# Kernel optimization log

Measured on AMD Instinct MI355X. Metric: run time of the kernel, lower is better.

## Reference

```python
import jax, jax.numpy as jnp
import numpy as np


def setup_inputs() -> dict:
    key = jax.random.key(0)
    k1, k2, k3, k4 = jax.random.split(key, 4)
    B, N, D, P = 1, 8192, 128, 2  # batch must be 1 (see .view(B,N,N) in source)
    x = jax.random.normal(k1, (B, N, D), dtype=jnp.float32)
    points = jax.random.normal(k2, (B, N, P), dtype=jnp.float32)
    # nn.Linear params, stored as (in, out) so y = x @ W + b
    W1 = jax.random.normal(k3, (2 * D, 2 * D), dtype=jnp.float32) * 0.04
    b1 = jnp.zeros((2 * D,), dtype=jnp.float32)
    W2 = jax.random.normal(k4, (2 * D, D), dtype=jnp.float32) * 0.04
    b2 = jnp.zeros((D,), dtype=jnp.float32)
    return {"x": x, "points": points, "W1": W1, "b1": b1, "W2": W2, "b2": b2, "K": 16}


def reference(x, points, W1, b1, W2, b2, K):
    B, N, _ = points.shape
    D = x.shape[-1]
    # torch.cdist on flattened (B*N, P) points, reshaped to (B, N, N)
    # (valid only for B == 1, matching the original module). Squared distance
    # is monotone in Euclidean distance, so top-k indices are identical.
    pf = points.reshape(B * N, -1)
    sq = jnp.sum(pf * pf, axis=-1)
    d2 = sq[:, None] + sq[None, :] - 2.0 * (pf @ pf.T)  # (BN, BN)
    d2 = d2.reshape(B, N, N)
    # topk(-dist, K+1) -> nearest K+1 (self first), drop self
    _, idx = jax.lax.top_k(-d2, K + 1)  # (B, N, K+1)
    idx = idx[:, :, 1:]  # (B, N, K)
    # gather neighbor features: knn_fts[b, n, k] = x[b, idx[b, n, k]]
    knn = x[jnp.arange(B)[:, None, None], idx]  # (B, N, K, D)
    center = jnp.broadcast_to(x[:, :, None, :], (B, N, K, D))
    local = jnp.concatenate([knn - center, center], axis=-1)  # (B, N, K, 2D)
    h = jax.nn.gelu(local @ W1 + b1, approximate=False)
    h = jax.nn.gelu(h @ W2 + b2, approximate=False)
    return jnp.mean(h, axis=2)  # (B, N, D)
```

## Files before the change

### kernel.cpp

```cpp
#include <hip/hip_runtime.h>

typedef __attribute__((ext_vector_type(8))) short short8;
typedef __attribute__((ext_vector_type(4))) float f32x4;

__device__ __forceinline__ unsigned short f2bf(float f) {
    unsigned int u = __float_as_uint(f);
    unsigned int r = u + 0x7fffu + ((u >> 16) & 1u);
    return (unsigned short)(r >> 16);
}

__device__ __forceinline__ float bf2f(short s) {
    return __uint_as_float(((unsigned int)(unsigned short)s) << 16);
}

__device__ __forceinline__ float gelu_fast(float v) {
    float x2 = v * v;
    float s  = v * fmaf(-0.102943195f, x2, -2.3022077f);
    float e  = __builtin_amdgcn_exp2f(s);
    return v * __builtin_amdgcn_rcpf(1.0f + e);
}

__device__ __forceinline__ unsigned int d2key(float d2) {
    unsigned int u = __float_as_uint(d2);
    return u ^ (((unsigned int)(((int)u) >> 31)) | 0x80000000u);
}

#define U64MAX 0xFFFFFFFFFFFFFFFFull

#define D2_FROM_Q(px, py, XI, YI, SQI)                                           \
    ({ const float sqj_ = __fadd_rn(__fmul_rn((px), (px)), __fmul_rn((py), (py))); \
       const float t_   = fmaf((YI), (py), __fmul_rn((XI), (px)));                 \
       const float s_   = __fadd_rn((SQI), sqj_);                                  \
       fmaf(-2.0f, t_, s_); })

__device__ __forceinline__ float bitonic64f(float v, int lane) {
#pragma unroll
    for (int k = 2; k <= 64; k <<= 1) {
#pragma unroll
        for (int j = k >> 1; j > 0; j >>= 1) {
            float pv = __shfl_xor(v, j, 64);
            const bool up  = ((lane & k) == 0);
            const bool low = ((lane & j) == 0);
            const float mn = fminf(v, pv);
            const float mx = fmaxf(v, pv);
            v = (up == low) ? mn : mx;
        }
    }
    return v;
}

__device__ __forceinline__ void insert_cand(
        unsigned long long* crow, int* cnt,
        float px, float py, float XI, float YI, float SQI, int i) {
    const float d2 = D2_FROM_Q(px, py, XI, YI, SQI);
    const unsigned int key = d2key(d2);
    int pos = atomicAdd(cnt, 1);
    if (pos < 128)
        crow[pos] = ((unsigned long long)key << 32) | (unsigned int)i;
}

#define KNN_SLACK 2.0e-3f

__global__ __launch_bounds__(256) void knn_kernel(
        const float* __restrict__ points,
        const float* __restrict__ W1, const float* __restrict__ W2,
        unsigned short* __restrict__ W1t, unsigned short* __restrict__ W2t,
        int* __restrict__ idx_out) {
    __shared__ float pmin[4][4][64];
    __shared__ float tshr[4];
    __shared__ unsigned long long cand[4][128];
    __shared__ int ccnt[4];

    const int bid = blockIdx.x;
    const int tid = threadIdx.x;

    if (bid < 384) {
        int g = bid * 256 + tid;
        if (g < 65536) {
            int d = g >> 8, c = g & 255;
            W1t[c * 256 + d] = f2bf(W1[g]);
        } else if (g < 98304) {
            int g2 = g - 65536;
            int d = g2 >> 7, c = g2 & 127;
            W2t[c * 256 + d] = f2bf(W2[g2]);
        }
        return;
    }

    const int wv    = tid >> 6;
    const int lane  = tid & 63;
    const int qbase = (bid - 384) << 2;

    float xi[4], yi[4], sqi_[4], n2x[4], n2y[4];
#pragma unroll
    for (int t = 0; t < 4; ++t) {
        xi[t] = points[(qbase + t) * 2 + 0];
        yi[t] = points[(qbase + t) * 2 + 1];
        sqi_[t] = __fadd_rn(__fmul_rn(xi[t], xi[t]), __fmul_rn(yi[t], yi[t]));
        n2x[t] = -2.0f * xi[t];
        n2y[t] = -2.0f * yi[t];
    }

    const float4* p4 = (const float4*)points;
    const float4* pw = p4 + wv * 1024 + lane;

    if (tid < 4) ccnt[tid] = 0;

    float vmn[4] = {1e30f, 1e30f, 1e30f, 1e30f};
#pragma unroll 4
    for (int j = 0; j < 16; ++j) {
        const float4 pp = pw[j * 64];
        const float sqa = fmaf(pp.x, pp.x, pp.y * pp.y);
        const float sqb = fmaf(pp.z, pp.z, pp.w * pp.w);
#pragma unroll
        for (int t = 0; t < 4; ++t) {
            const float da = fmaf(n2x[t], pp.x, fmaf(n2y[t], pp.y, sqa));
            const float db = fmaf(n2x[t], pp.z, fmaf(n2y[t], pp.w, sqb));
            vmn[t] = fminf(fminf(da, db), vmn[t]);
        }
    }
#pragma unroll
    for (int t = 0; t < 4; ++t) pmin[t][wv][lane] = vmn[t];
    __syncthreads();

    {
        const int q = wv;
        const float m = fminf(fminf(pmin[q][0][lane], pmin[q][1][lane]),
                              fminf(pmin[q][2][lane], pmin[q][3][lane]));
        const float s = bitonic64f(m, lane);
        if (lane == 16) tshr[q] = s + KNN_SLACK;
    }
    __syncthreads();
    float Ta[4];
#pragma unroll
    for (int t = 0; t < 4; ++t) Ta[t] = tshr[t];

#pragma unroll 4
    for (int j = 0; j < 16; ++j) {
        const float4 pp = pw[j * 64];
        const int i0 = (wv * 1024 + j * 64 + lane) * 2;
        const float sqa = fmaf(pp.x, pp.x, pp.y * pp.y);
        const float sqb = fmaf(pp.z, pp.z, pp.w * pp.w);
#pragma unroll
        for (int t = 0; t < 4; ++t) {
            const float da = fmaf(n2x[t], pp.x, fmaf(n2y[t], pp.y, sqa));
            const float db = fmaf(n2x[t], pp.z, fmaf(n2y[t], pp.w, sqb));
            if (fminf(da, db) <= Ta[t]) {
                if (da <= Ta[t])
                    insert_cand(cand[t], &ccnt[t],
                                pp.x, pp.y, xi[t], yi[t], sqi_[t], i0);
                if (db <= Ta[t])
                    insert_cand(cand[t], &ccnt[t],
                                pp.z, pp.w, xi[t], yi[t], sqi_[t], i0 + 1);
            }
        }
    }
    __syncthreads();

    {
        const int q = qbase + wv;
        const unsigned long long* candw = cand[wv];
        const int cc = ccnt[wv];
        const int n = cc < 128 ? cc : 128;
        const unsigned long long c0 = (lane < n)      ? candw[lane]      : U64MAX;
        const unsigned long long c1 = (lane + 64 < n) ? candw[lane + 64] : U64MAX;
        int r0 = 0, r1 = 0;
        for (int mI = 0; mI < n; ++mI) {
            const unsigned long long cm = candw[mI];
            r0 += (cm < c0) ? 1 : 0;
            r1 += (cm < c1) ? 1 : 0;
        }
        if (lane < n && r0 >= 1 && r0 <= 16)
            idx_out[q * 16 + r0 - 1] = (int)(unsigned int)(c0 & 0xFFFFFFFFull);
        if (lane + 64 < n && r1 >= 1 && r1 <= 16)
            idx_out[q * 16 + r1 - 1] = (int)(unsigned int)(c1 & 0xFFFFFFFFull);
    }
}

__global__ __launch_bounds__(256) void gemmAD_kernel(
        const float* __restrict__ x, const unsigned short* __restrict__ W1t,
        const float* __restrict__ b1,
        unsigned short* __restrict__ Abf, unsigned short* __restrict__ Dbf) {
    __shared__ unsigned short sx[64 * 136];
    __shared__ unsigned short tA[64 * 68];
    __shared__ unsigned short tD[64 * 68];
    const int tid = threadIdx.x;
    const int rb  = (blockIdx.x >> 2) * 64;
    const int cb  = (blockIdx.x & 3) * 64;

    {
        const int r   = ((tid >> 6) << 4) | (tid & 15);
        const int seg = (tid >> 4) & 3;
        const float* xr = x + (rb + r) * 128 + seg * 32;
        unsigned short* dst = sx + r * 136 + seg * 32;
#pragma unroll
        for (int u = 0; u < 8; ++u) {
            float4 a = ((const float4*)xr)[u];
            uint2 w;
            w.x = (unsigned)f2bf(a.x) | ((unsigned)f2bf(a.y) << 16);
            w.y = (unsigned)f2bf(a.z) | ((unsigned)f2bf(a.w) << 16);
            *(uint2*)(dst + u * 4) = w;
        }
    }
    __syncthreads();

    const int lane = tid & 63, wv = tid >> 6;
    const int m = lane & 15, quad = lane >> 4;
    const int ko0 = quad * 8;

    f32x4 accA[4], accC[4];
#pragma unroll
    for (int i = 0; i < 4; ++i) { accA[i] = (f32x4){0,0,0,0}; accC[i] = (f32x4){0,0,0,0}; }

    const int colL = wv * 16 + m;

#pragma unroll
    for (int ks = 0; ks < 4; ++ks) {
        const int ko = ks * 32 + ko0;
        short8 af[4];
#pragma unroll
        for (int rt = 0; rt < 4; ++rt)
            af[rt] = *(const short8*)(sx + (rt * 16 + m) * 136 + ko);
        const unsigned short* wp = W1t + (cb + colL) * 256 + ko;
        const short8 bA = *(const short8*)(wp);
        const short8 bC = *(const short8*)(wp + 128);
#pragma unroll
        for (int rt = 0; rt < 4; ++rt) {
            accA[rt] = __builtin_amdgcn_mfma_f32_16x16x32_bf16(af[rt], bA, accA[rt], 0, 0, 0);
            accC[rt] = __builtin_amdgcn_mfma_f32_16x16x32_bf16(af[rt], bC, accC[rt], 0, 0, 0);
        }
    }

    {
        const float bias = b1[cb + colL];
#pragma unroll
        for (int rt = 0; rt < 4; ++rt)
#pragma unroll
            for (int j = 0; j < 4; ++j) {
                const int rowL = rt * 16 + quad * 4 + j;
                float a = accA[rt][j];
                float d = accC[rt][j] - a + bias;
                tA[rowL * 68 + colL] = f2bf(a);
                tD[rowL * 68 + colL] = f2bf(d);
            }
    }
    __syncthreads();

    {
        const int r  = tid >> 2;
        const int sg = tid & 3;
        const unsigned short* sa = tA + r * 68 + sg * 16;
        const unsigned short* sd = tD + r * 68 + sg * 16;
        unsigned short* da = Abf + (rb + r) * 256 + cb + sg * 16;
        unsigned short* dd = Dbf + (rb + r) * 256 + cb + sg * 16;
        *(short8*)(da)     = *(const short8*)(sa);
        *(short8*)(da + 8) = *(const short8*)(sa + 8);
        *(short8*)(dd)     = *(const short8*)(sd);
        *(short8*)(dd + 8) = *(const short8*)(sd + 8);
    }
}

__global__ __launch_bounds__(256) void mlp_kernel(
        const unsigned short* __restrict__ Abf, const unsigned short* __restrict__ Dbf,
        const unsigned short* __restrict__ W2t, const float* __restrict__ b2,
        const int* __restrict__ idx, float* __restrict__ out) {
    __shared__ unsigned short sh[64 * 264];
    const int tid = threadIdx.x;
    const int qb  = blockIdx.x << 2;

    {
        const int r   = ((tid >> 6) << 4) | (tid & 15);
        const int seg = (tid >> 4) & 3;
        const int gq  = qb + (r >> 4);
        const int nb  = idx[(gq << 4) + (r & 15)];
        const unsigned short* arow = Abf + nb * 256 + seg * 64;
        const unsigned short* drow = Dbf + gq * 256 + seg * 64;
        unsigned short* dst = sh + r * 264 + seg * 64;
#pragma unroll
        for (int u = 0; u < 8; ++u) {
            short8 av = *(const short8*)(arow + u * 8);
            short8 dv = *(const short8*)(drow + u * 8);
            short8 hv;
#pragma unroll
            for (int e = 0; e < 8; ++e) {
                float h = bf2f(av[e]) + bf2f(dv[e]);
                hv[e] = (short)f2bf(gelu_fast(h));
            }
            *(short8*)(dst + u * 8) = hv;
        }
    }
    __syncthreads();

    const int lane = tid & 63, wv = tid >> 6;
    const int m = lane & 15, quad = lane >> 4;
    const int ko0 = quad * 8;

    f32x4 acc2[8];
#pragma unroll
    for (int i = 0; i < 8; ++i) acc2[i] = (f32x4){0.f, 0.f, 0.f, 0.f};
#pragma unroll
    for (int ks = 0; ks < 8; ++ks) {
        const int ko = ks * 32 + ko0;
        short8 af[4], bfr[2];
#pragma unroll
        for (int rt = 0; rt < 4; ++rt)
            af[rt] = *(const short8*)(sh + (rt * 16 + m) * 264 + ko);
#pragma unroll
        for (int ct = 0; ct < 2; ++ct)
            bfr[ct] = *(const short8*)(W2t + (wv * 32 + ct * 16 + m) * 256 + ko);
#pragma unroll
        for (int rt = 0; rt < 4; ++rt)
#pragma unroll
            for (int ct = 0; ct < 2; ++ct)
                acc2[rt * 2 + ct] = __builtin_amdgcn_mfma_f32_16x16x32_bf16(
                    af[rt], bfr[ct], acc2[rt * 2 + ct], 0, 0, 0);
    }

#pragma unroll
    for (int ct = 0; ct < 2; ++ct) {
        const int col = wv * 32 + ct * 16 + m;
        const float bias = b2[col];
#pragma unroll
        for (int rt = 0; rt < 4; ++rt) {
            float s = 0.f;
#pragma unroll
            for (int j = 0; j < 4; ++j)
                s += gelu_fast(acc2[rt * 2 + ct][j] + bias);
            s += __shfl_xor(s, 16, 64);
            s += __shfl_xor(s, 32, 64);
            if (quad == 0) out[(qb + rt) * 128 + col] = s * 0.0625f;
        }
    }
}

extern "C" void kernel_launch(void* const* d_in, const int* in_sizes, int n_in,
                              void* d_out, int out_size, void* d_ws, size_t ws_size,
                              hipStream_t stream) {
    const float* x      = (const float*)d_in[0];
    const float* points = (const float*)d_in[1];
    const float* W1     = (const float*)d_in[2];
    const float* b1     = (const float*)d_in[3];
    const float* W2     = (const float*)d_in[4];
    const float* b2     = (const float*)d_in[5];
    float* out = (float*)d_out;

    char* ws = (char*)d_ws;
    unsigned short* W1t = (unsigned short*)ws;
    unsigned short* W2t = (unsigned short*)(ws + 131072);
    int*            idx = (int*)(ws + 196608);
    unsigned short* Abf = (unsigned short*)(ws + 720896);
    unsigned short* Dbf = (unsigned short*)(ws + 4915200);

    knn_kernel<<<2432, 256, 0, stream>>>(points, W1, W2, W1t, W2t, idx);
    gemmAD_kernel<<<512, 256, 0, stream>>>(x, W1t, b1, Abf, Dbf);
    mlp_kernel<<<2048, 256, 0, stream>>>(Abf, Dbf, W2t, b2, idx, out);
}
```

Measured before the change: 131.5 us.

## Fuse first-layer GEMM into KNN kernel launch, reading W1 directly in fp32

Merges the x@W1 GEMM blocks into the KNN kernel as extra block ranges, removing one kernel launch and letting the GEMM run concurrently with the neighbor search. The W1 transpose-to-bf16 staging is dropped: each lane now gathers fp32 W1 elements with strided loads and converts them inline. Outputs are written straight to global memory without the shared-memory transpose, so stores are uncoalesced. The shared memory is reused across the block roles through a single union buffer.

```diff
diff --git a/kernel.cpp b/kernel.cpp
--- a/kernel.cpp
+++ b/kernel.cpp
@@ -61,35 +61,100 @@
 
 #define KNN_SLACK 2.0e-3f
 
-__global__ __launch_bounds__(256) void knn_kernel(
-        const float* __restrict__ points,
+__global__ __launch_bounds__(256) void fused_kernel(
+        const float* __restrict__ points, const float* __restrict__ x,
         const float* __restrict__ W1, const float* __restrict__ W2,
-        unsigned short* __restrict__ W1t, unsigned short* __restrict__ W2t,
+        const float* __restrict__ b1,
+        unsigned short* __restrict__ W2t,
+        unsigned short* __restrict__ Abf, unsigned short* __restrict__ Dbf,
         int* __restrict__ idx_out) {
-    __shared__ float pmin[4][4][64];
-    __shared__ float tshr[4];
-    __shared__ unsigned long long cand[4][128];
-    __shared__ int ccnt[4];
+    __shared__ unsigned long long smem8[2192];
 
     const int bid = blockIdx.x;
     const int tid = threadIdx.x;
 
-    if (bid < 384) {
-        int g = bid * 256 + tid;
-        if (g < 65536) {
-            int d = g >> 8, c = g & 255;
-            W1t[c * 256 + d] = f2bf(W1[g]);
-        } else if (g < 98304) {
-            int g2 = g - 65536;
-            int d = g2 >> 7, c = g2 & 127;
-            W2t[c * 256 + d] = f2bf(W2[g2]);
+    if (bid < 512) {
+        unsigned short* sx = (unsigned short*)smem8;
+        const int rb = (bid >> 2) * 64;
+        const int cb = (bid & 3) * 64;
+
+        {
+            const int r   = ((tid >> 6) << 4) | (tid & 15);
+            const int seg = (tid >> 4) & 3;
+            const float* xr = x + (rb + r) * 128 + seg * 32;
+            unsigned short* dst = sx + r * 136 + seg * 32;
+#pragma unroll
+            for (int u = 0; u < 8; ++u) {
+                float4 a = ((const float4*)xr)[u];
+                uint2 w;
+                w.x = (unsigned)f2bf(a.x) | ((unsigned)f2bf(a.y) << 16);
+                w.y = (unsigned)f2bf(a.z) | ((unsigned)f2bf(a.w) << 16);
+                *(uint2*)(dst + u * 4) = w;
+            }
+        }
+        __syncthreads();
+
+        const int lane = tid & 63, wv = tid >> 6;
+        const int m = lane & 15, quad = lane >> 4;
+        const int ko0 = quad * 8;
+
+        f32x4 accA[4], accC[4];
+#pragma unroll
+        for (int i = 0; i < 4; ++i) { accA[i] = (f32x4){0,0,0,0}; accC[i] = (f32x4){0,0,0,0}; }
+
+        const int gc = cb + wv * 16 + m;
+
+#pragma unroll
+        for (int ks = 0; ks < 4; ++ks) {
+            const int ko = ks * 32 + ko0;
+            short8 af[4];
+#pragma unroll
+            for (int rt = 0; rt < 4; ++rt)
+                af[rt] = *(const short8*)(sx + (rt * 16 + m) * 136 + ko);
+            short8 bA, bC;
+#pragma unroll
+            for (int e = 0; e < 8; ++e) {
+                bA[e] = (short)f2bf(W1[(ko + e) * 256 + gc]);
+                bC[e] = (short)f2bf(W1[(128 + ko + e) * 256 + gc]);
+            }
+#pragma unroll
+            for (int rt = 0; rt < 4; ++rt) {
+                accA[rt] = __builtin_amdgcn_mfma_f32_16x16x32_bf16(af[rt], bA, accA[rt], 0, 0, 0);
+                accC[rt] = __builtin_amdgcn_mfma_f32_16x16x32_bf16(af[rt], bC, accC[rt], 0, 0, 0);
+            }
+        }
+
+        {
+            const float bias = b1[gc];
+#pragma unroll
+            for (int rt = 0; rt < 4; ++rt)
+#pragma unroll
+                for (int j = 0; j < 4; ++j) {
+                    const int row = rb + rt * 16 + quad * 4 + j;
+                    float a = accA[rt][j];
+                    float d = accC[rt][j] - a + bias;
+                    Abf[row * 256 + gc] = f2bf(a);
+                    Dbf[row * 256 + gc] = f2bf(d);
+                }
         }
         return;
     }
+
+    if (bid < 640) {
+        int g = (bid - 512) * 256 + tid;
+        int d = g >> 7, c = g & 127;
+        W2t[c * 256 + d] = f2bf(W2[g]);
+        return;
+    }
+
+    unsigned long long (*cand)[128] = (unsigned long long(*)[128])smem8;
+    float (*pmin)[4][64] = (float(*)[4][64])(smem8 + 512);
+    float* tshr = (float*)(smem8 + 1024);
+    int*   ccnt = (int*)((char*)(smem8 + 1024) + 16);
 
     const int wv    = tid >> 6;
     const int lane  = tid & 63;
-    const int qbase = (bid - 384) << 2;
+    const int qbase = (bid - 640) << 2;
 
     float xi[4], yi[4], sqi_[4], n2x[4], n2y[4];
 #pragma unroll
@@ -177,89 +242,6 @@
     }
 }
 
-__global__ __launch_bounds__(256) void gemmAD_kernel(
-        const float* __restrict__ x, const unsigned short* __restrict__ W1t,
-        const float* __restrict__ b1,
-        unsigned short* __restrict__ Abf, unsigned short* __restrict__ Dbf) {
-    __shared__ unsigned short sx[64 * 136];
-    __shared__ unsigned short tA[64 * 68];
-    __shared__ unsigned short tD[64 * 68];
-    const int tid = threadIdx.x;
-    const int rb  = (blockIdx.x >> 2) * 64;
-    const int cb  = (blockIdx.x & 3) * 64;
-
-    {
-        const int r   = ((tid >> 6) << 4) | (tid & 15);
-        const int seg = (tid >> 4) & 3;
-        const float* xr = x + (rb + r) * 128 + seg * 32;
-        unsigned short* dst = sx + r * 136 + seg * 32;
-#pragma unroll
-        for (int u = 0; u < 8; ++u) {
-            float4 a = ((const float4*)xr)[u];
-            uint2 w;
-            w.x = (unsigned)f2bf(a.x) | ((unsigned)f2bf(a.y) << 16);
-            w.y = (unsigned)f2bf(a.z) | ((unsigned)f2bf(a.w) << 16);
-            *(uint2*)(dst + u * 4) = w;
-        }
-    }
-    __syncthreads();
-
-    const int lane = tid & 63, wv = tid >> 6;
-    const int m = lane & 15, quad = lane >> 4;
-    const int ko0 = quad * 8;
-
-    f32x4 accA[4], accC[4];
-#pragma unroll
-    for (int i = 0; i < 4; ++i) { accA[i] = (f32x4){0,0,0,0}; accC[i] = (f32x4){0,0,0,0}; }
-
-    const int colL = wv * 16 + m;
-
-#pragma unroll
-    for (int ks = 0; ks < 4; ++ks) {
-        const int ko = ks * 32 + ko0;
-        short8 af[4];
-#pragma unroll
-        for (int rt = 0; rt < 4; ++rt)
-            af[rt] = *(const short8*)(sx + (rt * 16 + m) * 136 + ko);
-        const unsigned short* wp = W1t + (cb + colL) * 256 + ko;
-        const short8 bA = *(const short8*)(wp);
-        const short8 bC = *(const short8*)(wp + 128);
-#pragma unroll
-        for (int rt = 0; rt < 4; ++rt) {
-            accA[rt] = __builtin_amdgcn_mfma_f32_16x16x32_bf16(af[rt], bA, accA[rt], 0, 0, 0);
-            accC[rt] = __builtin_amdgcn_mfma_f32_16x16x32_bf16(af[rt], bC, accC[rt], 0, 0, 0);
-        }
-    }
-
-    {
-        const float bias = b1[cb + colL];
-#pragma unroll
-        for (int rt = 0; rt < 4; ++rt)
-#pragma unroll
-            for (int j = 0; j < 4; ++j) {
-                const int rowL = rt * 16 + quad * 4 + j;
-                float a = accA[rt][j];
-                float d = accC[rt][j] - a + bias;
-                tA[rowL * 68 + colL] = f2bf(a);
-                tD[rowL * 68 + colL] = f2bf(d);
-            }
-    }
-    __syncthreads();
-
-    {
-        const int r  = tid >> 2;
-        const int sg = tid & 3;
-        const unsigned short* sa = tA + r * 68 + sg * 16;
-        const unsigned short* sd = tD + r * 68 + sg * 16;
-        unsigned short* da = Abf + (rb + r) * 256 + cb + sg * 16;
-        unsigned short* dd = Dbf + (rb + r) * 256 + cb + sg * 16;
-        *(short8*)(da)     = *(const short8*)(sa);
-        *(short8*)(da + 8) = *(const short8*)(sa + 8);
-        *(short8*)(dd)     = *(const short8*)(sd);
-        *(short8*)(dd + 8) = *(const short8*)(sd + 8);
-    }
-}
-
 __global__ __launch_bounds__(256) void mlp_kernel(
         const unsigned short* __restrict__ Abf, const unsigned short* __restrict__ Dbf,
         const unsigned short* __restrict__ W2t, const float* __restrict__ b2,
@@ -345,13 +327,11 @@
     float* out = (float*)d_out;
 
     char* ws = (char*)d_ws;
-    unsigned short* W1t = (unsigned short*)ws;
     unsigned short* W2t = (unsigned short*)(ws + 131072);
     int*            idx = (int*)(ws + 196608);
     unsigned short* Abf = (unsigned short*)(ws + 720896);
     unsigned short* Dbf = (unsigned short*)(ws + 4915200);
 
-    knn_kernel<<<2432, 256, 0, stream>>>(points, W1, W2, W1t, W2t, idx);
-    gemmAD_kernel<<<512, 256, 0, stream>>>(x, W1t, b1, Abf, Dbf);
+    fused_kernel<<<2688, 256, 0, stream>>>(points, x, W1, W2, b1, W2t, Abf, Dbf, idx);
     mlp_kernel<<<2048, 256, 0, stream>>>(Abf, Dbf, W2t, b2, idx, out);
 }
```

New measurement: 132.8 us. Within noise of the previous version (+0.9%).
